# Optimization experiments

Measured on AMD Instinct MI355X. Metric: run time of the kernel, lower is better.

The kernel has to match this reference:

```python
import jax, jax.numpy as jnp
import numpy as np

B, N_IN, N_HID, T = 64, 512, 512, 512


def setup_inputs() -> dict:
    key = jax.random.key(0)
    k1, k2, k3, k4, k5 = jax.random.split(key, 5)
    scale = 1.0 / np.sqrt(N_HID).astype(np.float32)
    return {
        "X": jax.random.normal(k1, (B, N_IN, T), dtype=jnp.float32),
        "Wax": jax.random.normal(k2, (N_IN, N_HID), dtype=jnp.float32) * scale,
        "Waa": jax.random.normal(k3, (N_HID, N_HID), dtype=jnp.float32) * scale,
        "bx": jax.random.normal(k4, (N_HID,), dtype=jnp.float32) * scale,
        "ba": jax.random.normal(k5, (N_HID,), dtype=jnp.float32) * scale,
    }


def reference(X, Wax, Waa, bx, ba):
    # X: [B, n_in, T]. a_{t+1} = tanh(x_t @ Wax + bx + a_t @ Waa + ba)
    # Precompute the input projections for all timesteps in one big GEMM:
    # [T, B, n_hid]
    Xt = jnp.transpose(X, (2, 0, 1))  # [T, B, n_in]
    inp_proj = jnp.einsum('tbi,ih->tbh', Xt, Wax) + bx + ba

    def step(a, u):
        a_next = jnp.tanh(u + a @ Waa)
        return a_next, a_next

    a0 = jnp.zeros((X.shape[0], Waa.shape[0]), dtype=X.dtype)
    _, A = jax.lax.scan(step, a0, inp_proj)
    return A  # [T, B, n_hid] == stacked A[1:] of the torch module
```

## Files before the change

kernel.cpp:

```cpp
#include <hip/hip_runtime.h>
#include <math.h>

#define BB   64
#define NIN  512
#define NH   512
#define TT   512

typedef _Float16 half2_t __attribute__((ext_vector_type(2)));
typedef _Float16 half8_t __attribute__((ext_vector_type(8)));
typedef float    f32x4  __attribute__((ext_vector_type(4)));

__device__ __forceinline__ unsigned pk16(float x, float y) {
    unsigned lo = (unsigned)__builtin_bit_cast(unsigned short, (_Float16)x);
    unsigned hi = (unsigned)__builtin_bit_cast(unsigned short, (_Float16)y);
    return lo | (hi << 16);
}

__device__ __forceinline__ float dot2u(unsigned w, unsigned a, float acc) {
    return __builtin_amdgcn_fdot2(__builtin_bit_cast(half2_t, w),
                                  __builtin_bit_cast(half2_t, a), acc, false);
}

__device__ __forceinline__ float tanh_fast(float x) {
    float ax = __builtin_fabsf(x);
    float e  = __builtin_amdgcn_exp2f(-2.885390082f * ax);
    float r  = (1.0f - e) * __builtin_amdgcn_rcpf(1.0f + e);
    return __builtin_copysignf(r, x);
}

__global__ __launch_bounds__(256) void inp_proj_mfma(
    const float* __restrict__ X, const float* __restrict__ Wax,
    const float* __restrict__ bx, const float* __restrict__ ba,
    float* __restrict__ out)
{
    __shared__ unsigned Xsp[16][132];
    __shared__ unsigned Wsp[16][132];

    const int b   = blockIdx.z;
    const int t0  = blockIdx.y * 128;
    const int h0  = blockIdx.x * 128;
    const int tid = threadIdx.x;
    const int lane = tid & 63;
    const int wid  = tid >> 6;
    const int wm   = wid >> 1;
    const int wn   = wid & 1;
    const int q    = lane >> 4;
    const int r16  = lane & 15;

    const int lr = tid >> 4;
    const int lc = (tid & 15) * 8;

    const float* Xb = X + (size_t)b * NIN * TT;

    f32x4 acc[4][4] = {};

    for (int i0 = 0; i0 < NIN; i0 += 32) {
        const int k0 = i0 + 2 * lr, k1 = k0 + 1;
        float4 xa0 = *(const float4*)&Xb[(size_t)k0 * TT + t0 + lc];
        float4 xa1 = *(const float4*)&Xb[(size_t)k0 * TT + t0 + lc + 4];
        float4 xb0 = *(const float4*)&Xb[(size_t)k1 * TT + t0 + lc];
        float4 xb1 = *(const float4*)&Xb[(size_t)k1 * TT + t0 + lc + 4];
        float4 wa0 = *(const float4*)&Wax[(size_t)k0 * NH + h0 + lc];
        float4 wa1 = *(const float4*)&Wax[(size_t)k0 * NH + h0 + lc + 4];
        float4 wb0 = *(const float4*)&Wax[(size_t)k1 * NH + h0 + lc];
        float4 wb1 = *(const float4*)&Wax[(size_t)k1 * NH + h0 + lc + 4];

        uint4 xp0, xp1, wp0, wp1;
        xp0.x = pk16(xa0.x, xb0.x); xp0.y = pk16(xa0.y, xb0.y);
        xp0.z = pk16(xa0.z, xb0.z); xp0.w = pk16(xa0.w, xb0.w);
        xp1.x = pk16(xa1.x, xb1.x); xp1.y = pk16(xa1.y, xb1.y);
        xp1.z = pk16(xa1.z, xb1.z); xp1.w = pk16(xa1.w, xb1.w);
        wp0.x = pk16(wa0.x, wb0.x); wp0.y = pk16(wa0.y, wb0.y);
        wp0.z = pk16(wa0.z, wb0.z); wp0.w = pk16(wa0.w, wb0.w);
        wp1.x = pk16(wa1.x, wb1.x); wp1.y = pk16(wa1.y, wb1.y);
        wp1.z = pk16(wa1.z, wb1.z); wp1.w = pk16(wa1.w, wb1.w);

        __syncthreads();
        *(uint4*)&Xsp[lr][lc]     = xp0;
        *(uint4*)&Xsp[lr][lc + 4] = xp1;
        *(uint4*)&Wsp[lr][lc]     = wp0;
        *(uint4*)&Wsp[lr][lc + 4] = wp1;
        __syncthreads();

        uint4 af[4], bf[4];
#pragma unroll
        for (int mt = 0; mt < 4; ++mt) {
            const int tc = wm * 64 + mt * 16 + r16;
            af[mt].x = Xsp[4 * q + 0][tc];
            af[mt].y = Xsp[4 * q + 1][tc];
            af[mt].z = Xsp[4 * q + 2][tc];
            af[mt].w = Xsp[4 * q + 3][tc];
        }
#pragma unroll
        for (int nt = 0; nt < 4; ++nt) {
            const int hc = wn * 64 + nt * 16 + r16;
            bf[nt].x = Wsp[4 * q + 0][hc];
            bf[nt].y = Wsp[4 * q + 1][hc];
            bf[nt].z = Wsp[4 * q + 2][hc];
            bf[nt].w = Wsp[4 * q + 3][hc];
        }
#pragma unroll
        for (int mt = 0; mt < 4; ++mt)
#pragma unroll
            for (int nt = 0; nt < 4; ++nt)
                acc[mt][nt] = __builtin_amdgcn_mfma_f32_16x16x32_f16(
                    __builtin_bit_cast(half8_t, af[mt]),
                    __builtin_bit_cast(half8_t, bf[nt]),
                    acc[mt][nt], 0, 0, 0);
    }

#pragma unroll
    for (int nt = 0; nt < 4; ++nt) {
        const int h = h0 + wn * 64 + nt * 16 + r16;
        const float bias = bx[h] + ba[h];
#pragma unroll
        for (int mt = 0; mt < 4; ++mt) {
            const int trow = t0 + wm * 64 + mt * 16 + q * 4;
#pragma unroll
            for (int rr = 0; rr < 4; ++rr) {
                out[(size_t)(trow + rr) * (BB * NH) + (size_t)b * NH + h] =
                    acc[mt][nt][rr] + bias;
            }
        }
    }
}

#define NRP 24
#define NLP 8
#define PSTRIDE 516

__device__ __forceinline__ unsigned bline(unsigned a, int l) {
    return (unsigned)__builtin_amdgcn_readlane((int)a, l);
}

__global__ __launch_bounds__(1024, 4) void rnn_scan_v6(
    const float* __restrict__ Waa, float* __restrict__ out)
{
    __shared__ uint4    wldsv[NLP][1024];
    __shared__ unsigned a_lds[2][256];
    __shared__ float    part[8][PSTRIDE];

    const int tid  = threadIdx.x;
    const int b    = blockIdx.x;
    const int cidx = tid & 127;
    const int kq   = tid >> 7;
    const int h4   = cidx * 4;
    const int l32  = tid & 31;

    unsigned w0[NRP], w1[NRP], w2[NRP], w3[NRP];
#pragma unroll
    for (int j = 0; j < NRP; ++j) {
        const int k = kq * 64 + 2 * j;
        float4 r0 = *(const float4*)&Waa[(size_t)k       * NH + h4];
        float4 r1 = *(const float4*)&Waa[(size_t)(k + 1) * NH + h4];
        w0[j] = pk16(r0.x, r1.x);
        w1[j] = pk16(r0.y, r1.y);
        w2[j] = pk16(r0.z, r1.z);
        w3[j] = pk16(r0.w, r1.w);
    }
#pragma unroll
    for (int p = 0; p < NLP; ++p) {
        const int k = kq * 64 + 2 * (NRP + p);
        float4 r0 = *(const float4*)&Waa[(size_t)k       * NH + h4];
        float4 r1 = *(const float4*)&Waa[(size_t)(k + 1) * NH + h4];
        uint4 wv;
        wv.x = pk16(r0.x, r1.x);
        wv.y = pk16(r0.y, r1.y);
        wv.z = pk16(r0.z, r1.z);
        wv.w = pk16(r0.w, r1.w);
        wldsv[p][tid] = wv;
    }

    if (tid < 256) a_lds[0][tid] = 0u;
    __syncthreads();

    const int  hc  = tid & 511;
    const bool red = (tid < 512);
    float* ob = out + (size_t)b * NH + hc;
    float u_cur = red ? ob[0] : 0.0f;

    for (int t = 0; t < TT; ++t) {
        const int tn = (t + 1 < TT) ? (t + 1) : (TT - 1);
        float u_next = red ? ob[(size_t)tn * (BB * NH)] : 0.0f;

        unsigned a_loc = a_lds[t & 1][kq * 32 + l32];

        float acc0 = 0.f, acc1 = 0.f, acc2 = 0.f, acc3 = 0.f;
#pragma unroll
        for (int j = 0; j < NRP; j += 2) {
            unsigned ra = bline(a_loc, j);
            unsigned rb = bline(a_loc, j + 1);
            acc0 = dot2u(w0[j], ra, acc0);
            acc1 = dot2u(w1[j], ra, acc1);
            acc2 = dot2u(w2[j], ra, acc2);
            acc3 = dot2u(w3[j], ra, acc3);
            acc0 = dot2u(w0[j + 1], rb, acc0);
            acc1 = dot2u(w1[j + 1], rb, acc1);
            acc2 = dot2u(w2[j + 1], rb, acc2);
            acc3 = dot2u(w3[j + 1], rb, acc3);
        }
#pragma unroll
        for (int p = 0; p < NLP; ++p) {
            unsigned ra = bline(a_loc, NRP + p);
            uint4 v = wldsv[p][tid];
            acc0 = dot2u(v.x, ra, acc0);
            acc1 = dot2u(v.y, ra, acc1);
            acc2 = dot2u(v.z, ra, acc2);
            acc3 = dot2u(v.w, ra, acc3);
        }

        float4 pv; pv.x = acc0; pv.y = acc1; pv.z = acc2; pv.w = acc3;
        *(float4*)&part[kq][h4] = pv;
        __builtin_amdgcn_s_waitcnt(0xC07F);
        __builtin_amdgcn_s_barrier();

        if (red) {
            float x = u_cur +
                (((part[0][hc] + part[1][hc]) + (part[2][hc] + part[3][hc])) +
                 ((part[4][hc] + part[5][hc]) + (part[6][hc] + part[7][hc])));
            float an = tanh_fast(x);
            ob[(size_t)t * (BB * NH)] = an;
            ((unsigned short*)a_lds[(t + 1) & 1])[hc] =
                __builtin_bit_cast(unsigned short, (_Float16)an);
        }
        u_cur = u_next;
        __builtin_amdgcn_s_waitcnt(0xC07F);
        __builtin_amdgcn_s_barrier();
    }
}

extern "C" void kernel_launch(void* const* d_in, const int* in_sizes, int n_in,
                              void* d_out, int out_size, void* d_ws, size_t ws_size,
                              hipStream_t stream) {
    const float* X   = (const float*)d_in[0];
    const float* Wax = (const float*)d_in[1];
    const float* Waa = (const float*)d_in[2];
    const float* bx  = (const float*)d_in[3];
    const float* ba  = (const float*)d_in[4];
    float* out = (float*)d_out;

    dim3 g1(NH / 128, TT / 128, BB);
    inp_proj_mfma<<<g1, 256, 0, stream>>>(X, Wax, bx, ba, out);
    rnn_scan_v6<<<BB, 1024, 0, stream>>>(Waa, out);
}
```

Measured before the change: 972.8 us.

## Remove second barrier per step via redundant per-wave reduction and double-buffered partials

Each wave now reduces the eight partial sums itself for the two hidden units it will broadcast, computes tanh, and keeps the fp16 packed state in a register. That removes the a_lds exchange and the second block barrier in every timestep, and the partial buffer is double-buffered so the next step's writes do not race with this step's reads. It also moves two more weight pairs from LDS into registers (NRP 26, NLP 6). The cost is redundant reduction and tanh work in both waves of each pair, plus higher register pressure, which could cause spills.

```diff
diff --git a/kernel.cpp b/kernel.cpp
--- a/kernel.cpp
+++ b/kernel.cpp
@@ -125,20 +125,18 @@
     }
 }
 
-#define NRP 24
-#define NLP 8
-#define PSTRIDE 516
+#define NRP 26
+#define NLP 6
 
 __device__ __forceinline__ unsigned bline(unsigned a, int l) {
     return (unsigned)__builtin_amdgcn_readlane((int)a, l);
 }
 
-__global__ __launch_bounds__(1024, 4) void rnn_scan_v6(
+__global__ __launch_bounds__(1024, 4) void rnn_scan_v7(
     const float* __restrict__ Waa, float* __restrict__ out)
 {
-    __shared__ uint4    wldsv[NLP][1024];
-    __shared__ unsigned a_lds[2][256];
-    __shared__ float    part[8][PSTRIDE];
+    __shared__ uint4 wldsv[NLP][1024];
+    __shared__ float part[2][8][512];
 
     const int tid  = threadIdx.x;
     const int b    = blockIdx.x;
@@ -146,6 +144,7 @@
     const int kq   = tid >> 7;
     const int h4   = cidx * 4;
     const int l32  = tid & 31;
+    const int wv   = tid >> 6;
 
     unsigned w0[NRP], w1[NRP], w2[NRP], w3[NRP];
 #pragma unroll
@@ -163,27 +162,24 @@
         const int k = kq * 64 + 2 * (NRP + p);
         float4 r0 = *(const float4*)&Waa[(size_t)k       * NH + h4];
         float4 r1 = *(const float4*)&Waa[(size_t)(k + 1) * NH + h4];
-        uint4 wv;
-        wv.x = pk16(r0.x, r1.x);
-        wv.y = pk16(r0.y, r1.y);
-        wv.z = pk16(r0.z, r1.z);
-        wv.w = pk16(r0.w, r1.w);
-        wldsv[p][tid] = wv;
-    }
-
-    if (tid < 256) a_lds[0][tid] = 0u;
+        uint4 wvv;
+        wvv.x = pk16(r0.x, r1.x);
+        wvv.y = pk16(r0.y, r1.y);
+        wvv.z = pk16(r0.z, r1.z);
+        wvv.w = pk16(r0.w, r1.w);
+        wldsv[p][tid] = wvv;
+    }
     __syncthreads();
 
-    const int  hc  = tid & 511;
-    const bool red = (tid < 512);
-    float* ob = out + (size_t)b * NH + hc;
-    float u_cur = red ? ob[0] : 0.0f;
+    const int h2 = kq * 64 + 2 * l32;
+    const float* ub = out + (size_t)b * NH + h2;
+    float2 u_cur = *(const float2*)ub;
+    unsigned a_loc = 0u;
+    const bool do_store = ((wv & 1) == 0);
 
     for (int t = 0; t < TT; ++t) {
         const int tn = (t + 1 < TT) ? (t + 1) : (TT - 1);
-        float u_next = red ? ob[(size_t)tn * (BB * NH)] : 0.0f;
-
-        unsigned a_loc = a_lds[t & 1][kq * 32 + l32];
+        float2 u_next = *(const float2*)&ub[(size_t)tn * (BB * NH)];
 
         float acc0 = 0.f, acc1 = 0.f, acc2 = 0.f, acc3 = 0.f;
 #pragma unroll
@@ -210,22 +206,31 @@
         }
 
         float4 pv; pv.x = acc0; pv.y = acc1; pv.z = acc2; pv.w = acc3;
-        *(float4*)&part[kq][h4] = pv;
+        *(float4*)&part[t & 1][kq][h4] = pv;
         __builtin_amdgcn_s_waitcnt(0xC07F);
         __builtin_amdgcn_s_barrier();
 
-        if (red) {
-            float x = u_cur +
-                (((part[0][hc] + part[1][hc]) + (part[2][hc] + part[3][hc])) +
-                 ((part[4][hc] + part[5][hc]) + (part[6][hc] + part[7][hc])));
-            float an = tanh_fast(x);
-            ob[(size_t)t * (BB * NH)] = an;
-            ((unsigned short*)a_lds[(t + 1) & 1])[hc] =
-                __builtin_bit_cast(unsigned short, (_Float16)an);
-        }
+        const float* pc = &part[t & 1][0][h2];
+        float2 s0 = *(const float2*)&pc[0 * 512];
+        float2 s1 = *(const float2*)&pc[1 * 512];
+        float2 s2 = *(const float2*)&pc[2 * 512];
+        float2 s3 = *(const float2*)&pc[3 * 512];
+        float2 s4 = *(const float2*)&pc[4 * 512];
+        float2 s5 = *(const float2*)&pc[5 * 512];
+        float2 s6 = *(const float2*)&pc[6 * 512];
+        float2 s7 = *(const float2*)&pc[7 * 512];
+        float x0 = u_cur.x + (((s0.x + s1.x) + (s2.x + s3.x)) +
+                              ((s4.x + s5.x) + (s6.x + s7.x)));
+        float x1 = u_cur.y + (((s0.y + s1.y) + (s2.y + s3.y)) +
+                              ((s4.y + s5.y) + (s6.y + s7.y)));
+        float an0 = tanh_fast(x0);
+        float an1 = tanh_fast(x1);
+        if (do_store) {
+            float2 st; st.x = an0; st.y = an1;
+            *(float2*)&out[(size_t)t * (BB * NH) + (size_t)b * NH + h2] = st;
+        }
+        a_loc = pk16(an0, an1);
         u_cur = u_next;
-        __builtin_amdgcn_s_waitcnt(0xC07F);
-        __builtin_amdgcn_s_barrier();
     }
 }
 
@@ -241,5 +246,5 @@
 
     dim3 g1(NH / 128, TT / 128, BB);
     inp_proj_mfma<<<g1, 256, 0, stream>>>(X, Wax, bx, ba, out);
-    rnn_scan_v6<<<BB, 1024, 0, stream>>>(Waa, out);
-}
+    rnn_scan_v7<<<BB, 1024, 0, stream>>>(Waa, out);
+}
```

After: 1.099 ms. 1.13x slower.
